# Performance work log

Measured on AMD Instinct MI355X. Metric: run time of the kernel, lower is better.

The kernel has to match this reference:

```python
import jax, jax.numpy as jnp
import numpy as np
import math

K = 3          # kernel_size
P_GEM = 3.0    # GeM power
EPS_GEM = 1e-6
EPS_NORM = 1e-12


def _l2n(x, axis):
    n = jnp.sqrt(jnp.sum(x * x, axis=axis, keepdims=True))
    return x / jnp.maximum(n, EPS_NORM)


def setup_inputs() -> dict:
    key = jax.random.key(0)
    ks = jax.random.split(key, 7)
    b, hw, c, nc = 32, 196, 768, 4096
    hidden = c  # mlp_ratio = 1
    return {
        "patch_tokens": jax.random.normal(ks[0], (b, hw, c), dtype=jnp.float32),
        "fc1_w": jax.random.normal(ks[1], (c, hidden), dtype=jnp.float32) * 0.02,
        "fc1_b": jnp.zeros((hidden,), dtype=jnp.float32),
        "fc2_w": jax.random.normal(ks[2], (hidden, c), dtype=jnp.float32) * 0.02,
        "fc2_b": jnp.zeros((c,), dtype=jnp.float32),
        "head_w": jax.random.normal(ks[3], (c, nc), dtype=jnp.float32) * 0.02,
        "head_b": jnp.zeros((nc,), dtype=jnp.float32),
    }


def reference(patch_tokens, fc1_w, fc1_b, fc2_w, fc2_b, head_w, head_b):
    b, hw, c = patch_tokens.shape
    h = w = int(math.sqrt(hw))

    # ---- SpaceSelfAware: pad -> unfold (3x3 local windows) -> multiply ----
    img = jnp.transpose(patch_tokens, (0, 2, 1)).reshape(b, c, h, w)
    # ZeroPad2d((left=1, right=1, top=2, bottom=0)) for kernel_size=3
    padded = jnp.pad(img, ((0, 0), (0, 0), (K - 1, 0), (K // 2, K // 2)))
    # stack the 9 shifted views, row-major over (ki, kj) matching nn.Unfold
    wins = jnp.stack(
        [padded[:, :, ki:ki + h, kj:kj + w] for ki in range(K) for kj in range(K)],
        axis=2,
    )  # (b, c, 9, h, w)
    y = wins.reshape(b, c, K, K, hw)
    y = jnp.transpose(y, (0, 4, 1, 2, 3))  # (b, hw, c, K, K)
    ssa = patch_tokens[:, :, :, None, None] * y  # (b, hw, c, K, K)

    # ---- space_fusion: L2Norm(dim=1) then GeM(p=3) over the KxK window ----
    ssa = _l2n(ssa, axis=1)
    pooled = jnp.mean(jnp.clip(ssa, EPS_GEM, None) ** P_GEM, axis=(-2, -1)) ** (1.0 / P_GEM)  # (b, hw, c)

    # ---- residual + L2 normalize over channels + Mlp ----
    tokens = pooled + patch_tokens
    tokens = _l2n(tokens, axis=-1)
    hdn = jax.nn.gelu(tokens @ fc1_w + fc1_b, approximate=False)
    tokens = hdn @ fc2_w + fc2_b  # (b, hw, c)

    # ---- GeMHead: GeM(p=3) over tokens, linear to nc, L2 normalize ----
    g = jnp.mean(jnp.clip(tokens, EPS_GEM, None) ** P_GEM, axis=1) ** (1.0 / P_GEM)  # (b, c)
    desc = g @ head_w + head_b  # (b, nc)
    desc = _l2n(desc, axis=-1)
    return desc
```

## Files before the change

kernel.cpp:

```cpp
#include <hip/hip_runtime.h>
#include <hip/hip_bf16.h>
#include <math.h>

#define B   32
#define P   196
#define C   768
#define NC  4096
#define HH  14
#define KSPLIT 12
#define NT  12
#define M6  6272
#define TW  (768 * 32)
#define TM  (M6 * 32)

typedef _Float16 half8 __attribute__((ext_vector_type(8)));
typedef _Float16 half4 __attribute__((ext_vector_type(4)));
typedef float f32x4 __attribute__((ext_vector_type(4)));

#define GLOAD_LDS16(g, l)                                                      \
    __builtin_amdgcn_global_load_lds(                                          \
        (const __attribute__((address_space(1))) void*)(g),                    \
        (__attribute__((address_space(3))) void*)(l), 16, 0, 0)

__global__ __launch_bounds__(256) void k_ssa(const float* __restrict__ t,
                                             _Float16* __restrict__ outP,
                                             float* __restrict__ spart,
                                             const float* __restrict__ W1,
                                             const float* __restrict__ W2,
                                             _Float16* __restrict__ O1,
                                             _Float16* __restrict__ O2) {
    __shared__ float xp_[256 * 16];
    __shared__ float part[4][9][16];
    __shared__ float inv_norm[9][16];
    __shared__ _Float16 outT[P][16];
    const int tid = threadIdx.x;

    if (blockIdx.z == 1) {
        const int idx = blockIdx.y * 48 + blockIdx.x;
        if (idx >= 1152) return;
        const bool second = idx >= 576;
        const int id2 = second ? idx - 576 : idx;
        const float* W = second ? W2 : W1;
        _Float16* WtP = second ? O2 : O1;
        const int kb = id2 / 24, nb2 = id2 % 24;
        const int k0 = kb * 32, n0 = nb2 * 32;
        float (*tt)[33] = (float (*)[33])xp_;
        const int r = tid / 32, c = tid % 32;
#pragma unroll
        for (int q = 0; q < 4; ++q)
            tt[r + q * 8][c] = W[(size_t)(k0 + r + q * 8) * C + n0 + c];
        __syncthreads();
        const int nl = tid >> 3, h = tid & 7;
        const int n = n0 + nl;
        half4 v;
#pragma unroll
        for (int j = 0; j < 4; ++j) v[j] = (_Float16)tt[h * 4 + j][nl];
        const int el = (h * 4) ^ (((n >> 1) & 3) << 3);
        *(half4*)&WtP[(size_t)kb * TW + (size_t)n * 32 + el] = v;
        return;
    }

    const int b = blockIdx.y, cb = blockIdx.x, c0 = cb * 16;
    const int cc = tid & 15, g = tid >> 4, wv = tid >> 6;

#pragma unroll
    for (int q = 0; q < 16; ++q) xp_[q * 256 + tid] = 0.0f;
    __syncthreads();

    for (int idx = tid; idx < 784; idx += 256) {
        const int p = idx >> 2, c = (idx & 3) * 4;
        const int i = p / HH, j = p % HH;
        *(float4*)&xp_[((i + 2) * 16 + (j + 1)) * 16 + c] =
            *(const float4*)&t[((size_t)b * P + p) * C + c0 + c];
    }
    __syncthreads();

    float s[9] = {};
    {
        int i = 0, j = g;
        if (j >= HH) { j -= HH; i = 1; }
        for (int p = g; p < P; p += 16) {
            const int base = ((i + 2) * 16 + (j + 1)) * 16 + cc;
            const float xp = xp_[base];
            const float xp2 = xp * xp;
#pragma unroll
            for (int k = 0; k < 9; ++k) {
                const int off = ((k / 3) - 2) * 16 + (k % 3) - 1;
                const float nb = xp_[base + off * 16];
                s[k] += xp2 * nb * nb;
            }
            j += 2; ++i;
            if (j >= HH) { j -= HH; ++i; }
        }
    }
#pragma unroll
    for (int k = 0; k < 9; ++k) {
        float r = s[k];
        r += __shfl_xor(r, 16);
        r += __shfl_xor(r, 32);
        s[k] = r;
    }
    if ((tid & 63) < 16) {
#pragma unroll
        for (int k = 0; k < 9; ++k) part[wv][k][cc] = s[k];
    }
    __syncthreads();
    if (tid < 144) {
        const int k = tid >> 4, c2 = tid & 15;
        const float t4 = part[0][k][c2] + part[1][k][c2] +
                         part[2][k][c2] + part[3][k][c2];
        inv_norm[k][c2] = 1.0f / fmaxf(sqrtf(t4), 1e-12f);
    }
    __syncthreads();

    float invn[9];
#pragma unroll
    for (int k = 0; k < 9; ++k) invn[k] = inv_norm[k][cc];

    {
        int i = 0, j = g;
        if (j >= HH) { j -= HH; i = 1; }
        for (int p = g; p < P; p += 16) {
            const int base = ((i + 2) * 16 + (j + 1)) * 16 + cc;
            const float xp = xp_[base];
            float acc = 0.0f;
#pragma unroll
            for (int k = 0; k < 9; ++k) {
                const int off = ((k / 3) - 2) * 16 + (k % 3) - 1;
                const float v = xp * xp_[base + off * 16];
                const float u = fmaxf(v * invn[k], 1e-6f);
                acc += u * u * u;
            }
            const float val = cbrtf(acc * (1.0f / 9.0f)) + xp;
            float rs = val * val;
            rs += __shfl_xor(rs, 1);
            rs += __shfl_xor(rs, 2);
            rs += __shfl_xor(rs, 4);
            rs += __shfl_xor(rs, 8);
            outT[p][cc] = (_Float16)val;
            if (cc == 0) spart[(size_t)cb * M6 + b * P + p] = rs;
            j += 2; ++i;
            if (j >= HH) { j -= HH; ++i; }
        }
    }
    __syncthreads();
    const int kb = cb >> 1, kbase = (cb & 1) * 16;
    for (int idx = tid; idx < P * 2; idx += 256) {
        const int p = idx >> 1, h = idx & 1;
        const half8 v = *(const half8*)&outT[p][h * 8];
        const int row = b * P + p;
        const int slot = ((kbase + h * 8) >> 3) ^ ((row >> 1) & 3);
        *(half8*)&outP[(size_t)kb * TM + (size_t)row * 32 + slot * 8] = v;
    }
}

template <bool GELU>
__global__ __launch_bounds__(256) void k_mfma_gemm(
    const _Float16* __restrict__ TokP,
    const _Float16* __restrict__ WtP,
    const float* __restrict__ bias,
    const float* __restrict__ spart,
    _Float16* __restrict__ Cout,
    float* __restrict__ gpart) {
    __shared__ _Float16 lA[3][2][64][32];
    __shared__ _Float16 lB[3][2][64][32];
    __shared__ float part2[2][2][64];
    __shared__ float invS[64];
    const int tid = threadIdx.x;
    const int w = tid >> 6, l = tid & 63;
    const int l15 = l & 15, lk = l >> 4;

    const int lid = blockIdx.x;
    int vm, vn;
    if (lid < 1152) { vm = (lid / 96) * 8 + (lid & 7); vn = (lid % 96) >> 3; }
    else            { const int r = lid - 1152; vm = 96 + r / 12; vn = r % 12; }
    const int m0 = vm * 64, n0 = vn * 64;
    const int wn = (w & 1) * 32, wm = (w >> 1) * 32;

    if constexpr (GELU) {
        if (tid < 64) {
            float s = 0.0f;
#pragma unroll 8
            for (int cb = 0; cb < 48; ++cb)
                s += spart[(size_t)cb * M6 + m0 + tid];
            invS[tid] = 1.0f / fmaxf(sqrtf(s), 1e-12f);
        }
        __syncthreads();
    }

    f32x4 acc[2][2] = {};

    const int kbsel = w & 1;
    const bool isB = (w >= 2);
    const _Float16* srcBase =
        isB ? (TokP + (size_t)m0 * 32) : (WtP + (size_t)n0 * 32);
    const size_t tileStride = isB ? (size_t)TM : (size_t)TW;
    _Float16* dst0 = isB ? &lB[0][kbsel][0][0] : &lA[0][kbsel][0][0];

#define ISSUE(tt, bf_)                                                         \
    {   const _Float16* s_ = srcBase + (size_t)(2 * (tt) + kbsel) * tileStride;\
        _Float16* d_ = dst0 + (size_t)(bf_) * 4096;                            \
        GLOAD_LDS16(s_ + l * 8,        d_ + l * 8);                            \
        GLOAD_LDS16(s_ + 512 + l * 8,  d_ + 512 + l * 8);                      \
        GLOAD_LDS16(s_ + 1024 + l * 8, d_ + 1024 + l * 8);                     \
        GLOAD_LDS16(s_ + 1536 + l * 8, d_ + 1536 + l * 8); }

    ISSUE(0, 0); ISSUE(1, 1); ISSUE(2, 2);

    for (int t = 0; t < NT; ++t) {
        if (t < NT - 2)       asm volatile("s_waitcnt vmcnt(8)" ::: "memory");
        else if (t == NT - 2) asm volatile("s_waitcnt vmcnt(4)" ::: "memory");
        else                  asm volatile("s_waitcnt vmcnt(0)" ::: "memory");
        __builtin_amdgcn_s_barrier();
        __builtin_amdgcn_sched_barrier(0);

        const int buf = t % 3;
#pragma unroll
        for (int kk = 0; kk < 2; ++kk) {
            half8 af[2], bf[2];
#pragma unroll
            for (int fa = 0; fa < 2; ++fa) {
                const int rowA = wn + fa * 16 + l15;
                const int colA = (lk ^ ((rowA >> 1) & 3)) * 8;
                af[fa] = *(const half8*)&lA[buf][kk][rowA][colA];
            }
#pragma unroll
            for (int fb = 0; fb < 2; ++fb) {
                const int rowB = wm + fb * 16 + l15;
                const int colB = (lk ^ ((rowB >> 1) & 3)) * 8;
                bf[fb] = *(const half8*)&lB[buf][kk][rowB][colB];
            }
#pragma unroll
            for (int fa = 0; fa < 2; ++fa)
#pragma unroll
                for (int fb = 0; fb < 2; ++fb)
                    acc[fa][fb] = __builtin_amdgcn_mfma_f32_16x16x32_f16(
                        af[fa], bf[fb], acc[fa][fb], 0, 0, 0);
        }
        asm volatile("s_waitcnt lgkmcnt(0)" ::: "memory");
        __builtin_amdgcn_s_barrier();
        __builtin_amdgcn_sched_barrier(0);
        if (t < NT - 3) ISSUE(t + 3, buf);
    }
#undef ISSUE

    const int b0 = m0 / P;
    const int rsplit = (b0 + 1) * P;
    float invm[2];
    if constexpr (GELU) {
#pragma unroll
        for (int fb = 0; fb < 2; ++fb)
            invm[fb] = invS[wm + fb * 16 + l15];
    }
#pragma unroll
    for (int fa = 0; fa < 2; ++fa) {
        const int nb = n0 + wn + fa * 16 + lk * 4;
        const float4 bv = *(const float4*)&bias[nb];
        if constexpr (GELU) {
#pragma unroll
            for (int fb = 0; fb < 2; ++fb) {
                const int m = m0 + wm + fb * 16 + l15;
                half4 o;
#pragma unroll
                for (int rr = 0; rr < 4; ++rr) {
                    float v = acc[fa][fb][rr] * invm[fb] + ((const float*)&bv)[rr];
                    v = 0.5f * v * (1.0f + erff(v * 0.70710678118654752f));
                    o[rr] = (_Float16)v;
                }
                const int el = (nb & 31) ^ (((m >> 1) & 3) << 3);
                *(half4*)&Cout[(size_t)(nb >> 5) * TM + (size_t)m * 32 + el] = o;
            }
        } else {
#pragma unroll
            for (int rr = 0; rr < 4; ++rr) {
                float s0 = 0.0f, s1 = 0.0f;
#pragma unroll
                for (int fb = 0; fb < 2; ++fb) {
                    const int m = m0 + wm + fb * 16 + l15;
                    const float v = acc[fa][fb][rr] + ((const float*)&bv)[rr];
                    const float u = fmaxf(v, 1e-6f);
                    const float u3 = u * u * u;
                    if (m >= rsplit) s1 += u3; else s0 += u3;
                }
                s0 += __shfl_xor(s0, 1); s0 += __shfl_xor(s0, 2);
                s0 += __shfl_xor(s0, 4); s0 += __shfl_xor(s0, 8);
                s1 += __shfl_xor(s1, 1); s1 += __shfl_xor(s1, 2);
                s1 += __shfl_xor(s1, 4); s1 += __shfl_xor(s1, 8);
                if (l15 == 0) {
                    part2[w >> 1][0][wn + fa * 16 + lk * 4 + rr] = s0;
                    part2[w >> 1][1][wn + fa * 16 + lk * 4 + rr] = s1;
                }
            }
        }
    }
    if constexpr (!GELU) {
        __syncthreads();
        if (tid < 128) {
            const int seg = tid >> 6, nn = tid & 63;
            const float tot = part2[0][seg][nn] + part2[1][seg][nn];
            if (seg == 0) {
                const int q = vm - ((b0 * 49) >> 4);
                gpart[((size_t)b0 * 4 + q) * C + n0 + nn] = tot;
            } else if (rsplit < m0 + 64) {
                gpart[((size_t)(b0 + 1) * 4 + 0) * C + n0 + nn] = tot;
            }
        }
    }
}

__global__ __launch_bounds__(256) void k_head1(const float* __restrict__ gpart,
                                               const float* __restrict__ W,
                                               float* __restrict__ partial) {
    const int n0 = blockIdx.x * 64;
    const int k0 = blockIdx.y * 64;
    __shared__ float gs[32][64];
    __shared__ float part[4][32][64];
    const int tid = threadIdx.x;

    for (int idx = tid; idx < 32 * 64; idx += 256) {
        const int b = idx >> 6, kk = idx & 63;
        const float* gp = &gpart[((size_t)b * 4) * C + k0 + kk];
        const float s = gp[0] + gp[C] + gp[2 * C] + gp[3 * C];
        gs[b][kk] = cbrtf(s * (1.0f / (float)P));
    }
    __syncthreads();

    const int c = tid & 63, q = tid >> 6;
    float acc[32] = {};
#pragma unroll
    for (int kk = 0; kk < 16; ++kk) {
        const int k = q * 16 + kk;
        const float wv = W[(size_t)(k0 + k) * NC + n0 + c];
#pragma unroll
        for (int b = 0; b < 32; ++b) acc[b] += gs[b][k] * wv;
    }
#pragma unroll
    for (int b = 0; b < 32; ++b) part[q][b][c] = acc[b];
    __syncthreads();

    for (int o = tid; o < 32 * 64; o += 256) {
        const int b = o >> 6, cc = o & 63;
        const float v = part[0][b][cc] + part[1][b][cc] +
                        part[2][b][cc] + part[3][b][cc];
        partial[((size_t)blockIdx.y * 32 + b) * NC + n0 + cc] = v;
    }
}

__global__ __launch_bounds__(256) void k_head2(const float* __restrict__ partial,
                                               const float* __restrict__ hb,
                                               float* __restrict__ out) {
    const int n = blockIdx.x * 256 + threadIdx.x;
    const int b = blockIdx.y;
    float s = hb[n];
#pragma unroll
    for (int ks = 0; ks < KSPLIT; ++ks)
        s += partial[((size_t)ks * 32 + b) * NC + n];
    out[(size_t)b * NC + n] = s;
}

__global__ __launch_bounds__(256) void k_outnorm(float* __restrict__ out) {
    const int b = blockIdx.x;
    float* r = out + (size_t)b * NC;
    const int tid = threadIdx.x;
    float v[16];
    float s = 0.0f;
#pragma unroll
    for (int q = 0; q < 16; ++q) {
        v[q] = r[tid + q * 256];
        s += v[q] * v[q];
    }
    __shared__ float partial[4];
    __shared__ float inv;
#pragma unroll
    for (int off = 32; off > 0; off >>= 1) s += __shfl_xor(s, off);
    if ((tid & 63) == 0) partial[tid >> 6] = s;
    __syncthreads();
    if (tid == 0)
        inv = 1.0f / fmaxf(sqrtf(partial[0] + partial[1] + partial[2] + partial[3]), 1e-12f);
    __syncthreads();
#pragma unroll
    for (int q = 0; q < 16; ++q) r[tid + q * 256] = v[q] * inv;
}

extern "C" void kernel_launch(void* const* d_in, const int* in_sizes, int n_in,
                              void* d_out, int out_size, void* d_ws, size_t ws_size,
                              hipStream_t stream) {
    const float* patch  = (const float*)d_in[0];
    const float* fc1_w  = (const float*)d_in[1];
    const float* fc1_b  = (const float*)d_in[2];
    const float* fc2_w  = (const float*)d_in[3];
    const float* fc2_b  = (const float*)d_in[4];
    const float* head_w = (const float*)d_in[5];
    const float* head_b = (const float*)d_in[6];
    float* out = (float*)d_out;

    const size_t big = (size_t)B * P * C;
    _Float16* tokU  = (_Float16*)d_ws;
    _Float16* hdnP  = tokU + big;
    _Float16* wt1   = hdnP + big;
    _Float16* wt2   = wt1 + C * C;
    float*    spart = (float*)(wt2 + C * C);
    float*    gpart = spart + 48 * (size_t)M6;
    float*    hpart = gpart + (size_t)B * 4 * C;

    k_ssa<<<dim3(48, B, 2), dim3(256), 0, stream>>>(
        patch, tokU, spart, fc1_w, fc2_w, wt1, wt2);
    k_mfma_gemm<true><<<dim3(1176), dim3(256), 0, stream>>>(
        tokU, wt1, fc1_b, spart, hdnP, nullptr);
    k_mfma_gemm<false><<<dim3(1176), dim3(256), 0, stream>>>(
        hdnP, wt2, fc2_b, nullptr, nullptr, gpart);
    k_head1<<<dim3(NC / 64, KSPLIT), dim3(256), 0, stream>>>(
        gpart, head_w, hpart);
    k_head2<<<dim3(NC / 256, B), dim3(256), 0, stream>>>(hpart, head_b, out);
    k_outnorm<<<dim3(B), dim3(256), 0, stream>>>(out);
}
```

Before: 82.01 us.

## Load weight fragments directly to registers and double-buffer only activations in LDS

The GEMM kernel stops staging the weight (A) tiles through LDS. Each wave now loads its weight fragments from the pre-swizzled global layout straight into registers, while only the token (B) tiles go through LDS, now double-buffered instead of triple-buffered. The loop is fully unrolled into ping-pong register sets with adjusted vmcnt waits, and launch bounds now request 4 blocks per CU. This cuts LDS footprint and LDS read traffic so occupancy can rise, at the cost of more registers and less prefetch depth for the B tiles.

```diff
diff --git a/kernel.cpp b/kernel.cpp
--- a/kernel.cpp
+++ b/kernel.cpp
@@ -155,15 +155,14 @@
 }
 
 template <bool GELU>
-__global__ __launch_bounds__(256) void k_mfma_gemm(
+__global__ __launch_bounds__(256, 4) void k_mfma_gemm(
     const _Float16* __restrict__ TokP,
     const _Float16* __restrict__ WtP,
     const float* __restrict__ bias,
     const float* __restrict__ spart,
     _Float16* __restrict__ Cout,
     float* __restrict__ gpart) {
-    __shared__ _Float16 lA[3][2][64][32];
-    __shared__ _Float16 lB[3][2][64][32];
+    __shared__ _Float16 lB[2][2][64][32];
     __shared__ float part2[2][2][64];
     __shared__ float invS[64];
     const int tid = threadIdx.x;
@@ -190,59 +189,78 @@
 
     f32x4 acc[2][2] = {};
 
-    const int kbsel = w & 1;
-    const bool isB = (w >= 2);
-    const _Float16* srcBase =
-        isB ? (TokP + (size_t)m0 * 32) : (WtP + (size_t)n0 * 32);
-    const size_t tileStride = isB ? (size_t)TM : (size_t)TW;
-    _Float16* dst0 = isB ? &lB[0][kbsel][0][0] : &lA[0][kbsel][0][0];
-
-#define ISSUE(tt, bf_)                                                         \
-    {   const _Float16* s_ = srcBase + (size_t)(2 * (tt) + kbsel) * tileStride;\
-        _Float16* d_ = dst0 + (size_t)(bf_) * 4096;                            \
-        GLOAD_LDS16(s_ + l * 8,        d_ + l * 8);                            \
-        GLOAD_LDS16(s_ + 512 + l * 8,  d_ + 512 + l * 8);                      \
-        GLOAD_LDS16(s_ + 1024 + l * 8, d_ + 1024 + l * 8);                     \
-        GLOAD_LDS16(s_ + 1536 + l * 8, d_ + 1536 + l * 8); }
-
-    ISSUE(0, 0); ISSUE(1, 1); ISSUE(2, 2);
-
-    for (int t = 0; t < NT; ++t) {
-        if (t < NT - 2)       asm volatile("s_waitcnt vmcnt(8)" ::: "memory");
-        else if (t == NT - 2) asm volatile("s_waitcnt vmcnt(4)" ::: "memory");
-        else                  asm volatile("s_waitcnt vmcnt(0)" ::: "memory");
+#define ISSUE_B(tt, st_)                                                       \
+    {   _Pragma("unroll")                                                      \
+        for (int qq = 0; qq < 2; ++qq) {                                       \
+            const int q = w * 2 + qq, kbp = q >> 2, ld = q & 3;                \
+            const _Float16* s_ = TokP + (size_t)(2 * (tt) + kbp) * TM +        \
+                                 (size_t)m0 * 32 + ld * 512;                   \
+            GLOAD_LDS16(s_ + l * 8, &lB[st_][kbp][ld * 16][0] + l * 8); }      }
+
+#define LOADA(dst, tt)                                                         \
+    {   _Pragma("unroll")                                                      \
+        for (int kk2 = 0; kk2 < 2; ++kk2)                                      \
+        _Pragma("unroll")                                                      \
+        for (int fa2 = 0; fa2 < 2; ++fa2) {                                    \
+            const int rowA = n0 + wn + fa2 * 16 + l15;                         \
+            dst[kk2 * 2 + fa2] = *(const half8*)&WtP[                          \
+                (size_t)(2 * (tt) + kk2) * TW + (size_t)rowA * 32 +            \
+                ((lk ^ ((rowA >> 1) & 3)) * 8)]; }                             }
+
+#define COMPUTE(st_, aR)                                                       \
+    {   _Pragma("unroll")                                                      \
+        for (int kk = 0; kk < 2; ++kk) {                                       \
+            half8 bf[2];                                                       \
+            _Pragma("unroll")                                                  \
+            for (int fb = 0; fb < 2; ++fb) {                                   \
+                const int rowB = wm + fb * 16 + l15;                           \
+                bf[fb] = *(const half8*)&lB[st_][kk][rowB]                     \
+                             [(lk ^ ((rowB >> 1) & 3)) * 8];                   \
+            }                                                                  \
+            _Pragma("unroll")                                                  \
+            for (int fa = 0; fa < 2; ++fa)                                     \
+            _Pragma("unroll")                                                  \
+            for (int fb = 0; fb < 2; ++fb)                                     \
+                acc[fa][fb] = __builtin_amdgcn_mfma_f32_16x16x32_f16(          \
+                    aR[kk * 2 + fa], bf[fb], acc[fa][fb], 0, 0, 0); }          }
+
+    half8 aW[4], aX[4];
+    ISSUE_B(0, 0);
+    __builtin_amdgcn_sched_barrier(0);
+    LOADA(aW, 0);
+    __builtin_amdgcn_sched_barrier(0);
+    ISSUE_B(1, 1);
+
+#pragma unroll
+    for (int tt = 0; tt < 6; ++tt) {
+        asm volatile("s_waitcnt vmcnt(6)" ::: "memory");
         __builtin_amdgcn_s_barrier();
         __builtin_amdgcn_sched_barrier(0);
-
-        const int buf = t % 3;
-#pragma unroll
-        for (int kk = 0; kk < 2; ++kk) {
-            half8 af[2], bf[2];
-#pragma unroll
-            for (int fa = 0; fa < 2; ++fa) {
-                const int rowA = wn + fa * 16 + l15;
-                const int colA = (lk ^ ((rowA >> 1) & 3)) * 8;
-                af[fa] = *(const half8*)&lA[buf][kk][rowA][colA];
-            }
-#pragma unroll
-            for (int fb = 0; fb < 2; ++fb) {
-                const int rowB = wm + fb * 16 + l15;
-                const int colB = (lk ^ ((rowB >> 1) & 3)) * 8;
-                bf[fb] = *(const half8*)&lB[buf][kk][rowB][colB];
-            }
-#pragma unroll
-            for (int fa = 0; fa < 2; ++fa)
-#pragma unroll
-                for (int fb = 0; fb < 2; ++fb)
-                    acc[fa][fb] = __builtin_amdgcn_mfma_f32_16x16x32_f16(
-                        af[fa], bf[fb], acc[fa][fb], 0, 0, 0);
-        }
+        COMPUTE(0, aW);
         asm volatile("s_waitcnt lgkmcnt(0)" ::: "memory");
         __builtin_amdgcn_s_barrier();
         __builtin_amdgcn_sched_barrier(0);
-        if (t < NT - 3) ISSUE(t + 3, buf);
-    }
-#undef ISSUE
+        LOADA(aX, 2 * tt + 1);
+        __builtin_amdgcn_sched_barrier(0);
+        if (tt < 5) ISSUE_B(2 * tt + 2, 0);
+
+        if (tt < 5) asm volatile("s_waitcnt vmcnt(6)" ::: "memory");
+        else        asm volatile("s_waitcnt vmcnt(4)" ::: "memory");
+        __builtin_amdgcn_s_barrier();
+        __builtin_amdgcn_sched_barrier(0);
+        COMPUTE(1, aX);
+        asm volatile("s_waitcnt lgkmcnt(0)" ::: "memory");
+        __builtin_amdgcn_s_barrier();
+        __builtin_amdgcn_sched_barrier(0);
+        if (tt < 5) {
+            LOADA(aW, 2 * tt + 2);
+            __builtin_amdgcn_sched_barrier(0);
+            ISSUE_B(2 * tt + 3, 1);
+        }
+    }
+#undef ISSUE_B
+#undef LOADA
+#undef COMPUTE
 
     const int b0 = m0 / P;
     const int rsplit = (b0 + 1) * P;
```

After: 81.82 us (median of 2 runs). About the same (-0.2%).
